# Performance work log

Measured on AMD Instinct MI355X. Metric: run time of the kernel, lower is better.

The kernel has to match this reference:

```python
import jax, jax.numpy as jnp
import numpy as np

RADIUS = 0.2
K = 32  # num_neighbors


def ball_query(centers, points, radius, k):
    """centers [B,3,M], points [B,3,N] -> int32 indices [B,M,k].
    Matches PointNet++ CUDA semantics: first k points (in original order)
    with squared distance < radius^2; slots beyond the count are filled
    with the first valid index (0 if no point is in the ball)."""
    cn = jnp.sum(centers * centers, axis=1)              # [B,M]
    pn = jnp.sum(points * points, axis=1)                # [B,N]
    cross = jnp.einsum('bdm,bdn->bmn', centers, points)  # [B,M,N]
    d2 = cn[:, :, None] + pn[:, None, :] - 2.0 * cross   # [B,M,N]
    valid = d2 < radius * radius
    # stable argsort puts valid indices first, preserving original order
    order = jnp.argsort(jnp.logical_not(valid), axis=-1, stable=True)
    idx = order[..., :k]                                  # [B,M,k]
    count = jnp.sum(valid, axis=-1, keepdims=True)        # [B,M,1]
    fill = idx[..., :1]                                   # first valid (or 0)
    return jnp.where(jnp.arange(k)[None, None, :] < count, idx, fill)


def group(features, idx):
    """features [B,C,N], idx [B,M,K] -> [B,C,M,K]."""
    return jax.vmap(lambda f, i: jnp.take(f, i, axis=1))(features, idx)


def setup_inputs() -> dict:
    key = jax.random.key(0)
    k1, k2, k3, k4 = jax.random.split(key, 4)
    B, N, M, C, CT = 8, 8192, 2048, 64, 64
    return {
        'points_coords': jax.random.uniform(k1, (B, 3, N), dtype=jnp.float32),
        'centers_coords': jax.random.uniform(k2, (B, 3, M), dtype=jnp.float32),
        'temb': jax.random.normal(k3, (B, CT, N), dtype=jnp.float32),
        'points_features': jax.random.normal(k4, (B, C, N), dtype=jnp.float32),
    }


def reference(points_coords, centers_coords, temb, points_features):
    idx = ball_query(centers_coords, points_coords, RADIUS, K)           # [B,M,K]
    neighbor_coords = group(points_coords, idx) - centers_coords[:, :, :, None]  # [B,3,M,K]
    neighbor_features = jnp.concatenate(
        [neighbor_coords, group(points_features, idx)], axis=1)          # [B,3+C,M,K]
    temb_grouped = group(temb, idx)                                      # [B,CT,M,K]
    return neighbor_features, temb_grouped
```

## Files before the change

kernel.cpp:

```cpp
#include <hip/hip_runtime.h>

#define B  8
#define N  8192
#define M  2048
#define C  64
#define CT 64
#define K  32
#define R2 0.04f

typedef __attribute__((ext_vector_type(4))) float f4;
typedef __attribute__((ext_vector_type(4))) int   i4;

__device__ __forceinline__ float rfl(float x) {
    union { float f; int i; } u;
    u.f = x;
    u.i = __builtin_amdgcn_readfirstlane(u.i);
    return u.f;
}

__global__ __launch_bounds__(256) void prep_points(
    const float* __restrict__ points,
    float* __restrict__ pointsT)
{
    const int b = blockIdx.x & 7;
    const int n = ((blockIdx.x >> 3) << 8) + threadIdx.x;
    const float* pc = points + (size_t)b * 3 * N;
    float* dst = pointsT + ((size_t)b * N + n) * 4;
    const float px = pc[n];
    const float py = pc[N + n];
    const float pz = pc[2 * N + n];
    dst[0] = px;
    dst[1] = py;
    dst[2] = pz;
    dst[3] = __fadd_rn(__fadd_rn(__fmul_rn(px, px), __fmul_rn(py, py)),
                       __fmul_rn(pz, pz));
}

#define PROC(vv, nn)                                                          \
    do {                                                                      \
        const float cross = __fadd_rn(                                        \
            __fadd_rn(__fmul_rn(cx, (vv).x), __fmul_rn(cy, (vv).y)),          \
            __fmul_rn(cz, (vv).z));                                           \
        const float d2 = __fsub_rn(__fadd_rn(cn, (vv).w),                     \
                                   __fmul_rn(2.0f, cross));                   \
        const bool valid = d2 < R2;                                           \
        const unsigned long long mask = __ballot(valid);                      \
        if (valid) {                                                          \
            const int slot = cnt + __builtin_amdgcn_mbcnt_hi(                 \
                (unsigned)(mask >> 32),                                       \
                __builtin_amdgcn_mbcnt_lo((unsigned)mask, 0));                \
            if (slot < K) snp[slot] = (nn);                                   \
        }                                                                     \
        cnt += (int)__popcll(mask);                                           \
    } while (0)

__global__ __launch_bounds__(256) void ballquery_kernel(
    const float* __restrict__ pointsT,
    const float* __restrict__ centers,
    int* __restrict__ idx,
    float* __restrict__ out1)
{
    __shared__ int sn[128];
    const int bid = blockIdx.x;
    const int b   = bid & 7;
    const int m0  = (bid >> 3) << 2;
    const int t    = threadIdx.x;
    const int wv   = t >> 6;
    const int lane = t & 63;
    const int m    = m0 + wv;

    const float cx = rfl(centers[((size_t)b * 3 + 0) * M + m]);
    const float cy = rfl(centers[((size_t)b * 3 + 1) * M + m]);
    const float cz = rfl(centers[((size_t)b * 3 + 2) * M + m]);
    const float cn = rfl(__fadd_rn(
        __fadd_rn(__fmul_rn(cx, cx), __fmul_rn(cy, cy)),
        __fmul_rn(cz, cz)));

    int* snp = &sn[wv * K];
    if (lane == 0) snp[0] = 0;

    const float4* pt4 = (const float4*)(pointsT + (size_t)b * N * 4);
    int cnt = 0;
    float4 va[4], vb[4];
    #pragma unroll
    for (int j = 0; j < 4; ++j) va[j] = pt4[j * 64 + lane];

    for (int g = 0; g < 32; g += 2) {
        if (g + 1 < 32) {
            #pragma unroll
            for (int j = 0; j < 4; ++j)
                vb[j] = pt4[((g + 1) * 4 + j) * 64 + lane];
        }
        #pragma unroll
        for (int j = 0; j < 4; ++j) PROC(va[j], g * 256 + j * 64 + lane);
        if (cnt >= K || g + 1 >= 32) break;

        if (g + 2 < 32) {
            #pragma unroll
            for (int j = 0; j < 4; ++j)
                va[j] = pt4[((g + 2) * 4 + j) * 64 + lane];
        }
        #pragma unroll
        for (int j = 0; j < 4; ++j) PROC(vb[j], (g + 1) * 256 + j * 64 + lane);
        if (cnt >= K) break;
    }

    if (lane < K) {
        const int fill = snp[0];
        const int v    = snp[lane];
        const int nf   = (lane < cnt) ? v : fill;
        idx[((size_t)b * M + m) * K + lane] = nf;

        const float4 p = *(const float4*)(pointsT + ((size_t)b * N + nf) * 4);
        const size_t cs = (size_t)M * K;
        const size_t o  = (size_t)b * 67 * cs + (size_t)m * K + lane;
        __builtin_nontemporal_store(p.x - cx, &out1[o]);
        __builtin_nontemporal_store(p.y - cy, &out1[o + cs]);
        __builtin_nontemporal_store(p.z - cz, &out1[o + 2 * cs]);
    }
}

__global__ __launch_bounds__(512) void gather_kernel(
    const float* __restrict__ temb,
    const float* __restrict__ feats,
    const int*   __restrict__ idx,
    float* __restrict__ out1,
    float* __restrict__ out2)
{
    __shared__ float row[2 * N];

    const int bid  = blockIdx.x;
    const int b    = bid & 7;
    const int slab = bid >> 3;
    const int tab  = slab >> 5;
    const int c0   = (slab & 31) * 2;
    const int t    = threadIdx.x;

    const f4* src4 = (const f4*)((tab ? temb : feats)
                                 + ((size_t)b * 64 + c0) * N);
    f4* lds4 = (f4*)row;
    #pragma unroll
    for (int i = 0; i < 8; ++i)
        lds4[i * 512 + t] = __builtin_nontemporal_load(&src4[i * 512 + t]);
    __syncthreads();

    const size_t cs = (size_t)M * K;
    float* o0 = tab ? (out2 + ((size_t)b * 64 + c0) * cs)
                    : (out1 + ((size_t)b * 67 + 3 + c0) * cs);
    f4* o0v = (f4*)o0;
    f4* o1v = (f4*)(o0 + cs);
    const i4* idx4 = (const i4*)(idx + (size_t)b * M * K);

    i4 nn = idx4[t];
    for (int it = 0; it < 32; ++it) {
        const int q = it * 512 + t;
        const i4 cur = nn;
        if (it < 31) nn = idx4[q + 512];
        f4 v0, v1;
        v0.x = row[cur.x];     v0.y = row[cur.y];
        v0.z = row[cur.z];     v0.w = row[cur.w];
        v1.x = row[N + cur.x]; v1.y = row[N + cur.y];
        v1.z = row[N + cur.z]; v1.w = row[N + cur.w];
        __builtin_nontemporal_store(v0, &o0v[q]);
        __builtin_nontemporal_store(v1, &o1v[q]);
    }
}

extern "C" void kernel_launch(void* const* d_in, const int* in_sizes, int n_in,
                              void* d_out, int out_size, void* d_ws, size_t ws_size,
                              hipStream_t stream) {
    const float* points  = (const float*)d_in[0];
    const float* centers = (const float*)d_in[1];
    const float* temb    = (const float*)d_in[2];
    const float* feats   = (const float*)d_in[3];

    float* pointsT = (float*)d_ws;
    int*   idxws   = (int*)(pointsT + (size_t)B * N * 4);

    float* out1 = (float*)d_out;
    float* out2 = out1 + (size_t)B * (3 + C) * M * K;

    prep_points<<<(B * N) / 256, 256, 0, stream>>>(points, pointsT);
    ballquery_kernel<<<(B * M) / 4, 256, 0, stream>>>(pointsT, centers,
                                                      idxws, out1);
    gather_kernel<<<B * 2 * 32, 512, 0, stream>>>(temb, feats, idxws,
                                                  out1, out2);
}
```

Before: 324.5 us.

## Fuse point preprocessing into ball query and stage points in LDS

Removes the separate prep_points kernel and its global float4 scratch buffer. Each ball-query block now loads the whole batch's point cloud into shared memory (x, y, z and squared norm) and runs 64 centers, 8 per wave, scanning points from LDS. This saves one launch and a global round-trip, and lets many centers reuse the same staged points. In exchange every block loads all N points even though the early exit usually needs only a fraction of them. The large LDS footprint also limits each CU to one block, which cuts the number of waves available to hide latency.

```diff
diff --git a/kernel.cpp b/kernel.cpp
--- a/kernel.cpp
+++ b/kernel.cpp
@@ -18,24 +18,6 @@
     return u.f;
 }
 
-__global__ __launch_bounds__(256) void prep_points(
-    const float* __restrict__ points,
-    float* __restrict__ pointsT)
-{
-    const int b = blockIdx.x & 7;
-    const int n = ((blockIdx.x >> 3) << 8) + threadIdx.x;
-    const float* pc = points + (size_t)b * 3 * N;
-    float* dst = pointsT + ((size_t)b * N + n) * 4;
-    const float px = pc[n];
-    const float py = pc[N + n];
-    const float pz = pc[2 * N + n];
-    dst[0] = px;
-    dst[1] = py;
-    dst[2] = pz;
-    dst[3] = __fadd_rn(__fadd_rn(__fmul_rn(px, px), __fmul_rn(py, py)),
-                       __fmul_rn(pz, pz));
-}
-
 #define PROC(vv, nn)                                                          \
     do {                                                                      \
         const float cross = __fadd_rn(                                        \
@@ -54,69 +36,80 @@
         cnt += (int)__popcll(mask);                                           \
     } while (0)
 
-__global__ __launch_bounds__(256) void ballquery_kernel(
-    const float* __restrict__ pointsT,
+__global__ __launch_bounds__(512) void ballquery_kernel(
+    const float* __restrict__ points,
     const float* __restrict__ centers,
     int* __restrict__ idx,
     float* __restrict__ out1)
 {
-    __shared__ int sn[128];
+    __shared__ float4 pts4[N];
+    __shared__ int    sn[64 * K];
+
     const int bid = blockIdx.x;
     const int b   = bid & 7;
-    const int m0  = (bid >> 3) << 2;
-    const int t    = threadIdx.x;
+    const int m0  = (bid >> 3) << 6;
+    const int t   = threadIdx.x;
+
+    {
+        const float* pc = points + (size_t)b * 3 * N;
+        #pragma unroll
+        for (int i = 0; i < 16; ++i) {
+            const int n = i * 512 + t;
+            const float px = pc[n];
+            const float py = pc[N + n];
+            const float pz = pc[2 * N + n];
+            float4 v;
+            v.x = px; v.y = py; v.z = pz;
+            v.w = __fadd_rn(__fadd_rn(__fmul_rn(px, px), __fmul_rn(py, py)),
+                            __fmul_rn(pz, pz));
+            pts4[n] = v;
+        }
+    }
+    __syncthreads();
+
     const int wv   = t >> 6;
     const int lane = t & 63;
-    const int m    = m0 + wv;
+    const size_t cs = (size_t)M * K;
 
-    const float cx = rfl(centers[((size_t)b * 3 + 0) * M + m]);
-    const float cy = rfl(centers[((size_t)b * 3 + 1) * M + m]);
-    const float cz = rfl(centers[((size_t)b * 3 + 2) * M + m]);
-    const float cn = rfl(__fadd_rn(
-        __fadd_rn(__fmul_rn(cx, cx), __fmul_rn(cy, cy)),
-        __fmul_rn(cz, cz)));
+    for (int k = 0; k < 8; ++k) {
+        const int ml = wv * 8 + k;
+        const int m  = m0 + ml;
 
-    int* snp = &sn[wv * K];
-    if (lane == 0) snp[0] = 0;
+        const float cx = rfl(centers[((size_t)b * 3 + 0) * M + m]);
+        const float cy = rfl(centers[((size_t)b * 3 + 1) * M + m]);
+        const float cz = rfl(centers[((size_t)b * 3 + 2) * M + m]);
+        const float cn = rfl(__fadd_rn(
+            __fadd_rn(__fmul_rn(cx, cx), __fmul_rn(cy, cy)),
+            __fmul_rn(cz, cz)));
 
-    const float4* pt4 = (const float4*)(pointsT + (size_t)b * N * 4);
-    int cnt = 0;
-    float4 va[4], vb[4];
-    #pragma unroll
-    for (int j = 0; j < 4; ++j) va[j] = pt4[j * 64 + lane];
+        int* snp = &sn[ml * K];
+        if (lane == 0) snp[0] = 0;
+        int cnt = 0;
 
-    for (int g = 0; g < 32; g += 2) {
-        if (g + 1 < 32) {
-            #pragma unroll
-            for (int j = 0; j < 4; ++j)
-                vb[j] = pt4[((g + 1) * 4 + j) * 64 + lane];
+        for (int c = 0; c < 128; c += 4) {
+            const float4 v0 = pts4[(c + 0) * 64 + lane];
+            const float4 v1 = pts4[(c + 1) * 64 + lane];
+            const float4 v2 = pts4[(c + 2) * 64 + lane];
+            const float4 v3 = pts4[(c + 3) * 64 + lane];
+            PROC(v0, (c + 0) * 64 + lane);
+            PROC(v1, (c + 1) * 64 + lane);
+            PROC(v2, (c + 2) * 64 + lane);
+            PROC(v3, (c + 3) * 64 + lane);
+            if (cnt >= K) break;
         }
-        #pragma unroll
-        for (int j = 0; j < 4; ++j) PROC(va[j], g * 256 + j * 64 + lane);
-        if (cnt >= K || g + 1 >= 32) break;
 
-        if (g + 2 < 32) {
-            #pragma unroll
-            for (int j = 0; j < 4; ++j)
-                va[j] = pt4[((g + 2) * 4 + j) * 64 + lane];
+        if (lane < K) {
+            const int fill = snp[0];
+            const int v    = snp[lane];
+            const int nf   = (lane < cnt) ? v : fill;
+            idx[((size_t)b * M + m) * K + lane] = nf;
+
+            const float4 p = pts4[nf];
+            const size_t o = (size_t)b * 67 * cs + (size_t)m * K + lane;
+            __builtin_nontemporal_store(p.x - cx, &out1[o]);
+            __builtin_nontemporal_store(p.y - cy, &out1[o + cs]);
+            __builtin_nontemporal_store(p.z - cz, &out1[o + 2 * cs]);
         }
-        #pragma unroll
-        for (int j = 0; j < 4; ++j) PROC(vb[j], (g + 1) * 256 + j * 64 + lane);
-        if (cnt >= K) break;
-    }
-
-    if (lane < K) {
-        const int fill = snp[0];
-        const int v    = snp[lane];
-        const int nf   = (lane < cnt) ? v : fill;
-        idx[((size_t)b * M + m) * K + lane] = nf;
-
-        const float4 p = *(const float4*)(pointsT + ((size_t)b * N + nf) * 4);
-        const size_t cs = (size_t)M * K;
-        const size_t o  = (size_t)b * 67 * cs + (size_t)m * K + lane;
-        __builtin_nontemporal_store(p.x - cx, &out1[o]);
-        __builtin_nontemporal_store(p.y - cy, &out1[o + cs]);
-        __builtin_nontemporal_store(p.z - cz, &out1[o + 2 * cs]);
     }
 }
 
@@ -174,15 +167,13 @@
     const float* temb    = (const float*)d_in[2];
     const float* feats   = (const float*)d_in[3];
 
-    float* pointsT = (float*)d_ws;
-    int*   idxws   = (int*)(pointsT + (size_t)B * N * 4);
+    int* idxws = (int*)d_ws;
 
     float* out1 = (float*)d_out;
     float* out2 = out1 + (size_t)B * (3 + C) * M * K;
 
-    prep_points<<<(B * N) / 256, 256, 0, stream>>>(points, pointsT);
-    ballquery_kernel<<<(B * M) / 4, 256, 0, stream>>>(pointsT, centers,
-                                                      idxws, out1);
+    ballquery_kernel<<<B * (M / 64), 512, 0, stream>>>(points, centers,
+                                                       idxws, out1);
     gather_kernel<<<B * 2 * 32, 512, 0, stream>>>(temb, feats, idxws,
                                                   out1, out2);
 }
```

After: 328.8 us. No clear change (+1.3%).
